# Optimization experiments

Measured on AMD Instinct MI355X. Metric: run time of the kernel, lower is better.

Reference implementation:

```python
import jax, jax.numpy as jnp
import numpy as np

H = 8
DH = 64
MAX_REL = 32
SCALE = DH ** -0.5


def setup_inputs() -> dict:
    key = jax.random.key(0)
    ks = jax.random.split(key, 10)
    B, T, D = 2, 2048, 512
    s = 1.0 / np.sqrt(D)
    return {
        "hidden_states": jax.random.normal(ks[0], (B, T, D), jnp.float32),
        "Wq": jax.random.normal(ks[1], (D, H * DH), jnp.float32) * s,
        "bq": jax.random.normal(ks[2], (H * DH,), jnp.float32) * 0.02,
        "Wk": jax.random.normal(ks[3], (D, H * DH), jnp.float32) * s,
        "bk": jax.random.normal(ks[4], (H * DH,), jnp.float32) * 0.02,
        "Wv": jax.random.normal(ks[5], (D, H * DH), jnp.float32) * s,
        "bv": jax.random.normal(ks[6], (H * DH,), jnp.float32) * 0.02,
        "Wo": jax.random.normal(ks[7], (H * DH, D), jnp.float32) * s,
        "bo": jax.random.normal(ks[8], (D,), jnp.float32) * 0.02,
        "rel_bias": jax.random.normal(ks[9], (H, 2 * MAX_REL + 1), jnp.float32) * 0.02,
    }


def _rel_pos_bias(rel_bias, Tq, Tk):
    # (H, Tq, Tk) additive bias from clamped relative distances
    rel = jnp.arange(Tq)[:, None] - jnp.arange(Tk)[None, :]
    idx = jnp.clip(rel, -MAX_REL, MAX_REL) + MAX_REL
    return rel_bias[:, idx]


def reference(hidden_states, Wq, bq, Wk, bk, Wv, bv, Wo, bo, rel_bias):
    B, T, D = hidden_states.shape
    # projections (enn.Linear == dense linear map in forward math)
    Q = (hidden_states @ Wq + bq).reshape(B, T, H, DH)
    K = (hidden_states @ Wk + bk).reshape(B, T, H, DH)
    V = (hidden_states @ Wv + bv).reshape(B, T, H, DH)
    attn = jnp.einsum("bthd,bkhd->bhtk", Q, K) * SCALE
    attn = attn + _rel_pos_bias(rel_bias, T, T)[None]
    attn = jax.nn.softmax(attn, axis=-1)
    out = jnp.einsum("bhtk,bkhd->bthd", attn, V).reshape(B, T, H * DH)
    return out @ Wo + bo
```

## Files before the change

kernel.cpp:

```cpp
#include <hip/hip_runtime.h>
#include <stdint.h>
#include <math.h>

#define H 8
#define DH 64
#define T 2048
#define D 512
#define B 2
#define BH 16
#define MAXREL 32
#define NREL (2*MAXREL+1)
#define C1 0.18033688f
#define NW (D*D)

typedef _Float16 half_t;
typedef half_t half8 __attribute__((ext_vector_type(8)));
typedef half_t half4 __attribute__((ext_vector_type(4)));
typedef float f32x4 __attribute__((ext_vector_type(4)));
typedef int int4v __attribute__((ext_vector_type(4)));

typedef __attribute__((address_space(3))) unsigned int lds_uint;
typedef const __attribute__((address_space(1))) unsigned int glb_uint;

__device__ __forceinline__ void gl_lds16(const void* g, void* l) {
    __builtin_amdgcn_global_load_lds((glb_uint*)g, (lds_uint*)l, 16, 0, 0);
}
__device__ __forceinline__ f32x4 zero4() { f32x4 z = {0.f,0.f,0.f,0.f}; return z; }
__device__ __forceinline__ int pkrtz(float a, float b) {
    return __builtin_bit_cast(int, __builtin_amdgcn_cvt_pkrtz(a, b));
}

__global__ __launch_bounds__(256) void prep(
    const float* __restrict__ X,
    const float* __restrict__ Wq, const float* __restrict__ Wk,
    const float* __restrict__ Wv, const float* __restrict__ Wo,
    half_t* __restrict__ Xh, half_t* __restrict__ Wts)
{
    __shared__ half_t Ld[64 * 72];
    const int bid = blockIdx.x;
    const int tid = threadIdx.x;
    if (bid < 1024) {
        const int i = (bid * 256 + tid) * 8;
        const float4 a = *(const float4*)(X + i);
        const float4 b = *(const float4*)(X + i + 4);
        half8 o;
        o[0]=(half_t)a.x; o[1]=(half_t)a.y; o[2]=(half_t)a.z; o[3]=(half_t)a.w;
        o[4]=(half_t)b.x; o[5]=(half_t)b.y; o[6]=(half_t)b.z; o[7]=(half_t)b.w;
        *(half8*)(Xh + i) = o;
    } else {
        const int id = bid - 1024;
        const int z = id >> 6;
        const int tile = id & 63;
        const float* __restrict__ W = (z==0)?Wq:(z==1)?Wk:(z==2)?Wv:Wo;
        half_t* __restrict__ out = Wts + (size_t)z * NW;
        const int k0 = (tile >> 3) * 64;
        const int n0 = (tile & 7) * 64;
        const int r = tid >> 2, c16 = (tid & 3) * 16;
        const float* src = W + (size_t)(k0 + r) * D + n0 + c16;
        #pragma unroll
        for (int j = 0; j < 16; ++j) Ld[r * 72 + c16 + j] = (half_t)src[j];
        __syncthreads();
        half_t tmp[16];
        #pragma unroll
        for (int j = 0; j < 16; ++j) tmp[j] = Ld[(c16 + j) * 72 + r];
        half8* dst = (half8*)(out + (size_t)(n0 + r) * D + k0 + c16);
        dst[0] = *(half8*)&tmp[0];
        dst[1] = *(half8*)&tmp[8];
    }
}

__global__ __launch_bounds__(256) void gemm_qkv(
    const half_t* __restrict__ Xh, const half_t* __restrict__ Wts,
    const float* __restrict__ bq, const float* __restrict__ bk,
    const float* __restrict__ bv,
    half_t* __restrict__ Qh, half_t* __restrict__ Kh, half_t* __restrict__ Vth)
{
    __shared__ half_t As[2][64 * 64];
    __shared__ half_t Bs[2][128 * 64];
    const int tid = threadIdx.x, w = tid >> 6, lane = tid & 63;
    const int l15 = lane & 15, quad = lane >> 4;
    const int m0 = blockIdx.x * 64, n0 = blockIdx.y * 128, z = blockIdx.z;
    const half_t* __restrict__ Wt = Wts + (size_t)z * NW;
    const float* __restrict__ bias = (z==0)?bq:(z==1)?bk:bv;

    auto stage = [&](int buf, int k0) {
        #pragma unroll
        for (int s = 0; s < 2; ++s) {
            const int cid = (w * 2 + s) * 64 + lane;
            const int r = cid >> 3, c = (cid & 7) ^ (r & 7);
            gl_lds16(Xh + (size_t)(m0 + r) * D + k0 + c * 8,
                     &As[buf][(w * 2 + s) * 512]);
        }
        #pragma unroll
        for (int s = 0; s < 4; ++s) {
            const int cid = (w * 4 + s) * 64 + lane;
            const int r = cid >> 3, c = (cid & 7) ^ (r & 7);
            gl_lds16(Wt + (size_t)(n0 + r) * D + k0 + c * 8,
                     &Bs[buf][(w * 4 + s) * 512]);
        }
    };

    f32x4 acc[4][2];
    #pragma unroll
    for (int ms = 0; ms < 4; ++ms) { acc[ms][0] = zero4(); acc[ms][1] = zero4(); }

    stage(0, 0);
    __syncthreads();
    for (int it = 0; it < 8; ++it) {
        const int cur = it & 1;
        if (it < 7) stage(cur ^ 1, (it + 1) * 64);
        const int swiz = l15 & 7;
        #pragma unroll
        for (int ks = 0; ks < 2; ++ks) {
            const int c = (ks * 4 + quad) ^ swiz;
            half8 bf[2];
            #pragma unroll
            for (int nt = 0; nt < 2; ++nt)
                bf[nt] = *(const half8*)&Bs[cur][(w * 32 + nt * 16 + l15) * 64 + c * 8];
            #pragma unroll
            for (int ms = 0; ms < 4; ++ms) {
                const half8 af = *(const half8*)&As[cur][(ms * 16 + l15) * 64 + c * 8];
                acc[ms][0] = __builtin_amdgcn_mfma_f32_16x16x32_f16(af, bf[0], acc[ms][0], 0, 0, 0);
                acc[ms][1] = __builtin_amdgcn_mfma_f32_16x16x32_f16(af, bf[1], acc[ms][1], 0, 0, 0);
            }
        }
        __syncthreads();
    }

    float bvv[2];
    #pragma unroll
    for (int nt = 0; nt < 2; ++nt) bvv[nt] = bias[n0 + w * 32 + nt * 16 + l15];

    if (z == 2) {
        #pragma unroll
        for (int ms = 0; ms < 4; ++ms) {
            const int mbase = m0 + ms * 16 + quad * 4;
            const int bb = mbase >> 11, t0 = mbase & 2047;
            #pragma unroll
            for (int nt = 0; nt < 2; ++nt) {
                const int n = n0 + w * 32 + nt * 16 + l15;
                const int hh = n >> 6, d = n & 63;
                half4 pk;
                #pragma unroll
                for (int r = 0; r < 4; ++r) pk[r] = (half_t)(acc[ms][nt][r] + bvv[nt]);
                *(half4*)(Vth + (((size_t)bb * H + hh) * DH + d) * T + t0) = pk;
            }
        }
    } else {
        half_t* __restrict__ dst = (z == 0) ? Qh : Kh;
        #pragma unroll
        for (int ms = 0; ms < 4; ++ms)
            #pragma unroll
            for (int nt = 0; nt < 2; ++nt)
                #pragma unroll
                for (int r = 0; r < 4; ++r) {
                    const int mrow = m0 + ms * 16 + quad * 4 + r;
                    const int n = n0 + w * 32 + nt * 16 + l15;
                    const int bb = mrow >> 11, t = mrow & 2047, hh = n >> 6, d = n & 63;
                    dst[(((size_t)bb * H + hh) * T + t) * DH + d] = (half_t)(acc[ms][nt][r] + bvv[nt]);
                }
    }
}

__global__ __launch_bounds__(256) void attn_fwd(
    const half_t* __restrict__ Qh, const half_t* __restrict__ Kh,
    const half_t* __restrict__ Vth, const float* __restrict__ relb,
    half_t* __restrict__ Onum, half_t* __restrict__ lsum)
{
    __shared__ half_t Kt[2][4096];
    __shared__ half_t Vt[2][4096];
    __shared__ float rb2[NREL];

    const int tid = threadIdx.x, w = tid >> 6, lane = tid & 63;
    const int l15 = lane & 15, quad = lane >> 4;
    const int q0 = blockIdx.x * 64;
    const int qw = q0 + w * 16;
    const int bh = blockIdx.y;
    const int split = blockIdx.z;
    const int kb0 = split * 1024;
    const int h = bh & 7;

    if (tid < NREL) rb2[tid] = relb[h * NREL + tid] * 1.44269504f;

    half8 qf[2];
    const half_t* Qbase = Qh + ((size_t)bh * T + qw) * DH;
    #pragma unroll
    for (int ks = 0; ks < 2; ++ks)
        qf[ks] = *(const half8*)(Qbase + l15 * DH + ks * 32 + quad * 8);

    f32x4 of[4];
    #pragma unroll
    for (int nt = 0; nt < 4; ++nt) of[nt] = zero4();
    float lp = 0.f;

    auto stage = [&](int buf, int kb) {
        #pragma unroll
        for (int s = 0; s < 2; ++s) {
            const int cid = (w * 2 + s) * 64 + lane;
            const int r = cid >> 3, cg = (cid & 7) ^ (r & 7);
            gl_lds16(Kh + ((size_t)bh * T + kb + r) * DH + cg * 8,
                     &Kt[buf][(w * 2 + s) * 512]);
            gl_lds16(Vth + ((size_t)bh * DH + r) * T + kb + cg * 8,
                     &Vt[buf][(w * 2 + s) * 512]);
        }
    };

    stage(0, kb0);
    __syncthreads();

    const int qg = qw + l15;
    const int swiz = l15 & 7;

    for (int it = 0; it < 16; ++it) {
        const int cur = it & 1;
        if (it + 1 < 16) stage(cur ^ 1, kb0 + (it + 1) * 64);
        const int kb = kb0 + it * 64;

        f32x4 st[4];
        #pragma unroll
        for (int nt = 0; nt < 4; ++nt) st[nt] = zero4();
        #pragma unroll
        for (int ks = 0; ks < 2; ++ks) {
            const int c = (ks * 4 + quad) ^ swiz;
            #pragma unroll
            for (int nt = 0; nt < 4; ++nt) {
                const half8 kf = *(const half8*)&Kt[cur][(nt * 16 + l15) * 64 + c * 8];
                st[nt] = __builtin_amdgcn_mfma_f32_16x16x32_f16(kf, qf[ks], st[nt], 0, 0, 0);
            }
        }

        int pd[4][2];
        const bool uni_hi = (qw - (kb + 63)) >= MAXREL;
        const bool uni_lo = ((qw + 15) - kb) <= -MAXREL;
        if (uni_hi || uni_lo) {
            const float bu = uni_hi ? rb2[NREL - 1] : rb2[0];
            #pragma unroll
            for (int nt = 0; nt < 4; ++nt) {
                float p[4];
                #pragma unroll
                for (int r = 0; r < 4; ++r) p[r] = exp2f(fmaf(st[nt][r], C1, bu));
                lp += (p[0] + p[1]) + (p[2] + p[3]);
                pd[nt][0] = pkrtz(p[0], p[1]);
                pd[nt][1] = pkrtz(p[2], p[3]);
            }
        } else {
            #pragma unroll
            for (int nt = 0; nt < 4; ++nt) {
                float p[4];
                #pragma unroll
                for (int r = 0; r < 4; ++r) {
                    const int key = kb + nt * 16 + quad * 4 + r;
                    int rel = qg - key;
                    rel = rel < -MAXREL ? -MAXREL : (rel > MAXREL ? MAXREL : rel);
                    p[r] = exp2f(fmaf(st[nt][r], C1, rb2[rel + MAXREL]));
                }
                lp += (p[0] + p[1]) + (p[2] + p[3]);
                pd[nt][0] = pkrtz(p[0], p[1]);
                pd[nt][1] = pkrtz(p[2], p[3]);
            }
        }

        #pragma unroll
        for (int ks = 0; ks < 2; ++ks) {
            int4v bd;
            #pragma unroll
            for (int d = 0; d < 4; ++d) {
                const int src = ((quad & 1) * 2 + (d >> 1)) * 16 + l15;
                const int va = __shfl(pd[2 * ks][d & 1], src);
                const int vb = __shfl(pd[2 * ks + 1][d & 1], src);
                bd[d] = (quad >> 1) ? vb : va;
            }
            const half8 pf = __builtin_bit_cast(half8, bd);
            const int c = (ks * 4 + quad) ^ swiz;
            #pragma unroll
            for (int nt = 0; nt < 4; ++nt) {
                const half8 vf = *(const half8*)&Vt[cur][(nt * 16 + l15) * 64 + c * 8];
                of[nt] = __builtin_amdgcn_mfma_f32_16x16x32_f16(vf, pf, of[nt], 0, 0, 0);
            }
        }
        __syncthreads();
    }

    const size_t qrow = (size_t)(split * BH + bh) * T + qw + l15;
    half_t* obase = Onum + qrow * DH;
    #pragma unroll
    for (int nt = 0; nt < 4; ++nt) {
        half4 pk;
        #pragma unroll
        for (int r = 0; r < 4; ++r) pk[r] = (half_t)(of[nt][r] * 0.015625f);
        *(half4*)(obase + nt * 16 + quad * 4) = pk;
    }
    lp += __shfl_xor(lp, 16);
    lp += __shfl_xor(lp, 32);
    if (quad == 0) lsum[qrow] = (half_t)(lp * 0.015625f);
}

__global__ __launch_bounds__(256) void combine(
    const half_t* __restrict__ Onum, const half_t* __restrict__ lsum,
    half_t* __restrict__ AOh)
{
    const int i = blockIdx.x * 256 + threadIdx.x;
    const int r = i >> 6;
    const int c = (i & 63) * 8;
    const int b = r >> 11, t = r & 2047, hh = c >> 6, d = c & 63;
    const int bh = b * H + hh;
    const size_t o0 = ((size_t)bh * T + t) * DH + d;
    const size_t o1 = ((size_t)(BH + bh) * T + t) * DH + d;
    const half8 x0 = *(const half8*)(Onum + o0);
    const half8 x1 = *(const half8*)(Onum + o1);
    const float l = (float)lsum[(size_t)bh * T + t] + (float)lsum[(size_t)(BH + bh) * T + t];
    const float inv = 1.0f / l;
    half8 o;
    #pragma unroll
    for (int j = 0; j < 8; ++j) o[j] = (half_t)(((float)x0[j] + (float)x1[j]) * inv);
    *(half8*)(AOh + (size_t)r * D + c) = o;
}

__global__ __launch_bounds__(256) void gemm_out(
    const half_t* __restrict__ AOh, const half_t* __restrict__ Wot,
    const float* __restrict__ bo, float* __restrict__ out)
{
    __shared__ half_t As[2][32 * 64];
    __shared__ half_t Bs[2][128 * 64];
    const int tid = threadIdx.x, w = tid >> 6, lane = tid & 63;
    const int l15 = lane & 15, quad = lane >> 4;
    const int m0 = blockIdx.x * 32, n0 = blockIdx.y * 128;

    auto stage = [&](int buf, int k0) {
        {
            const int cid = w * 64 + lane;
            const int r = cid >> 3, c = (cid & 7) ^ (r & 7);
            gl_lds16(AOh + (size_t)(m0 + r) * D + k0 + c * 8,
                     &As[buf][w * 512]);
        }
        #pragma unroll
        for (int s = 0; s < 4; ++s) {
            const int cid = (w * 4 + s) * 64 + lane;
            const int r = cid >> 3, c = (cid & 7) ^ (r & 7);
            gl_lds16(Wot + (size_t)(n0 + r) * D + k0 + c * 8,
                     &Bs[buf][(w * 4 + s) * 512]);
        }
    };

    f32x4 acc[2][2];
    #pragma unroll
    for (int ms = 0; ms < 2; ++ms) { acc[ms][0] = zero4(); acc[ms][1] = zero4(); }

    stage(0, 0);
    __syncthreads();
    for (int it = 0; it < 8; ++it) {
        const int cur = it & 1;
        if (it < 7) stage(cur ^ 1, (it + 1) * 64);
        const int swiz = l15 & 7;
        #pragma unroll
        for (int ks = 0; ks < 2; ++ks) {
            const int c = (ks * 4 + quad) ^ swiz;
            half8 bf[2];
            #pragma unroll
            for (int nt = 0; nt < 2; ++nt)
                bf[nt] = *(const half8*)&Bs[cur][(w * 32 + nt * 16 + l15) * 64 + c * 8];
            #pragma unroll
            for (int ms = 0; ms < 2; ++ms) {
                const half8 af = *(const half8*)&As[cur][(ms * 16 + l15) * 64 + c * 8];
                acc[ms][0] = __builtin_amdgcn_mfma_f32_16x16x32_f16(af, bf[0], acc[ms][0], 0, 0, 0);
                acc[ms][1] = __builtin_amdgcn_mfma_f32_16x16x32_f16(af, bf[1], acc[ms][1], 0, 0, 0);
            }
        }
        __syncthreads();
    }

    float bvv[2];
    #pragma unroll
    for (int nt = 0; nt < 2; ++nt) bvv[nt] = bo[n0 + w * 32 + nt * 16 + l15];
    #pragma unroll
    for (int ms = 0; ms < 2; ++ms)
        #pragma unroll
        for (int nt = 0; nt < 2; ++nt)
            #pragma unroll
            for (int r = 0; r < 4; ++r) {
                const int mrow = m0 + ms * 16 + quad * 4 + r;
                const int n = n0 + w * 32 + nt * 16 + l15;
                out[(size_t)mrow * D + n] = acc[ms][nt][r] + bvv[nt];
            }
}

extern "C" void kernel_launch(void* const* d_in, const int* in_sizes, int n_in,
                              void* d_out, int out_size, void* d_ws, size_t ws_size,
                              hipStream_t stream)
{
    const float* hs   = (const float*)d_in[0];
    const float* Wq   = (const float*)d_in[1];
    const float* bq   = (const float*)d_in[2];
    const float* Wk   = (const float*)d_in[3];
    const float* bk   = (const float*)d_in[4];
    const float* Wv   = (const float*)d_in[5];
    const float* bv   = (const float*)d_in[6];
    const float* Wo   = (const float*)d_in[7];
    const float* bo   = (const float*)d_in[8];
    const float* relb = (const float*)d_in[9];

    const size_t NX = (size_t)B * T * D;
    half_t* wsh = (half_t*)d_ws;
    half_t* Xh  = wsh;
    half_t* Wts = Xh + NX;
    half_t* Qh  = Wts + 4 * (size_t)NW;
    half_t* Kh  = Qh + NX;
    half_t* Vth = Kh + NX;
    half_t* On  = Vth + NX;
    half_t* Ls  = On + 2 * NX;
    half_t* AOh = Ls + 2 * BH * T;

    prep    <<<dim3(1280), 256, 0, stream>>>(hs, Wq, Wk, Wv, Wo, Xh, Wts);
    gemm_qkv<<<dim3(64, 4, 3), 256, 0, stream>>>(Xh, Wts, bq, bk, bv, Qh, Kh, Vth);
    attn_fwd<<<dim3(32, BH, 2), 256, 0, stream>>>(Qh, Kh, Vth, relb, On, Ls);
    combine <<<dim3(1024), 256, 0, stream>>>(On, Ls, AOh);
    gemm_out<<<dim3(128, 4), 256, 0, stream>>>(AOh, Wts + 3 * (size_t)NW, bo, (float*)d_out);
}
```

Before: 147.4 us.

## Process two query tiles per wave and split keys four ways in attention

Each wave now handles 32 query rows (two 16-row groups), so every K/V fragment read from LDS feeds two MFMAs. This cuts LDS traffic per unit of work. The key dimension is split four ways instead of two, which keeps the grid at the same 1024 blocks. Partial outputs go to two buffers, one of which reuses the output buffer, and the combine kernel reads the input-cast buffer as its destination. In exchange, register pressure rises under the new occupancy hint, and the combine step has more partials to read.

```diff
diff --git a/kernel.cpp b/kernel.cpp
--- a/kernel.cpp
+++ b/kernel.cpp
@@ -12,6 +12,8 @@
 #define NREL (2*MAXREL+1)
 #define C1 0.18033688f
 #define NW (D*D)
+#define NSPLIT 4
+#define NKIT (T/NSPLIT/64)
 
 typedef _Float16 half_t;
 typedef half_t half8 __attribute__((ext_vector_type(8)));
@@ -162,10 +164,11 @@
     }
 }
 
-__global__ __launch_bounds__(256) void attn_fwd(
+__global__ __launch_bounds__(256, 4) void attn_fwd(
     const half_t* __restrict__ Qh, const half_t* __restrict__ Kh,
     const half_t* __restrict__ Vth, const float* __restrict__ relb,
-    half_t* __restrict__ Onum, half_t* __restrict__ lsum)
+    half_t* __restrict__ On01, half_t* __restrict__ On23,
+    half_t* __restrict__ lsum)
 {
     __shared__ half_t Kt[2][4096];
     __shared__ half_t Vt[2][4096];
@@ -173,25 +176,28 @@
 
     const int tid = threadIdx.x, w = tid >> 6, lane = tid & 63;
     const int l15 = lane & 15, quad = lane >> 4;
-    const int q0 = blockIdx.x * 64;
-    const int qw = q0 + w * 16;
+    const int qw = blockIdx.x * 128 + w * 32;
     const int bh = blockIdx.y;
     const int split = blockIdx.z;
-    const int kb0 = split * 1024;
+    const int kb0 = split * (T / NSPLIT);
     const int h = bh & 7;
 
     if (tid < NREL) rb2[tid] = relb[h * NREL + tid] * 1.44269504f;
 
-    half8 qf[2];
+    half8 qf[2][2];
     const half_t* Qbase = Qh + ((size_t)bh * T + qw) * DH;
     #pragma unroll
-    for (int ks = 0; ks < 2; ++ks)
-        qf[ks] = *(const half8*)(Qbase + l15 * DH + ks * 32 + quad * 8);
-
-    f32x4 of[4];
-    #pragma unroll
-    for (int nt = 0; nt < 4; ++nt) of[nt] = zero4();
-    float lp = 0.f;
+    for (int g = 0; g < 2; ++g)
+        #pragma unroll
+        for (int ks = 0; ks < 2; ++ks)
+            qf[g][ks] = *(const half8*)(Qbase + (g * 16 + l15) * DH + ks * 32 + quad * 8);
+
+    f32x4 of[2][4];
+    #pragma unroll
+    for (int g = 0; g < 2; ++g)
+        #pragma unroll
+        for (int nt = 0; nt < 4; ++nt) of[g][nt] = zero4();
+    float lp[2] = {0.f, 0.f};
 
     auto stage = [&](int buf, int kb) {
         #pragma unroll
@@ -208,111 +214,137 @@
     stage(0, kb0);
     __syncthreads();
 
-    const int qg = qw + l15;
     const int swiz = l15 & 7;
 
-    for (int it = 0; it < 16; ++it) {
+    for (int it = 0; it < NKIT; ++it) {
         const int cur = it & 1;
-        if (it + 1 < 16) stage(cur ^ 1, kb0 + (it + 1) * 64);
+        if (it + 1 < NKIT) stage(cur ^ 1, kb0 + (it + 1) * 64);
         const int kb = kb0 + it * 64;
 
-        f32x4 st[4];
-        #pragma unroll
-        for (int nt = 0; nt < 4; ++nt) st[nt] = zero4();
+        f32x4 st[2][4];
+        #pragma unroll
+        for (int g = 0; g < 2; ++g)
+            #pragma unroll
+            for (int nt = 0; nt < 4; ++nt) st[g][nt] = zero4();
         #pragma unroll
         for (int ks = 0; ks < 2; ++ks) {
             const int c = (ks * 4 + quad) ^ swiz;
             #pragma unroll
             for (int nt = 0; nt < 4; ++nt) {
                 const half8 kf = *(const half8*)&Kt[cur][(nt * 16 + l15) * 64 + c * 8];
-                st[nt] = __builtin_amdgcn_mfma_f32_16x16x32_f16(kf, qf[ks], st[nt], 0, 0, 0);
-            }
-        }
-
-        int pd[4][2];
+                st[0][nt] = __builtin_amdgcn_mfma_f32_16x16x32_f16(kf, qf[0][ks], st[0][nt], 0, 0, 0);
+                st[1][nt] = __builtin_amdgcn_mfma_f32_16x16x32_f16(kf, qf[1][ks], st[1][nt], 0, 0, 0);
+            }
+        }
+
+        int pd[2][4][2];
         const bool uni_hi = (qw - (kb + 63)) >= MAXREL;
-        const bool uni_lo = ((qw + 15) - kb) <= -MAXREL;
+        const bool uni_lo = ((qw + 31) - kb) <= -MAXREL;
         if (uni_hi || uni_lo) {
             const float bu = uni_hi ? rb2[NREL - 1] : rb2[0];
             #pragma unroll
-            for (int nt = 0; nt < 4; ++nt) {
-                float p[4];
+            for (int g = 0; g < 2; ++g)
                 #pragma unroll
-                for (int r = 0; r < 4; ++r) p[r] = exp2f(fmaf(st[nt][r], C1, bu));
-                lp += (p[0] + p[1]) + (p[2] + p[3]);
-                pd[nt][0] = pkrtz(p[0], p[1]);
-                pd[nt][1] = pkrtz(p[2], p[3]);
-            }
+                for (int nt = 0; nt < 4; ++nt) {
+                    float p[4];
+                    #pragma unroll
+                    for (int r = 0; r < 4; ++r) p[r] = exp2f(fmaf(st[g][nt][r], C1, bu));
+                    lp[g] += (p[0] + p[1]) + (p[2] + p[3]);
+                    pd[g][nt][0] = pkrtz(p[0], p[1]);
+                    pd[g][nt][1] = pkrtz(p[2], p[3]);
+                }
         } else {
             #pragma unroll
-            for (int nt = 0; nt < 4; ++nt) {
-                float p[4];
+            for (int g = 0; g < 2; ++g) {
+                const int qg = qw + g * 16 + l15;
                 #pragma unroll
-                for (int r = 0; r < 4; ++r) {
-                    const int key = kb + nt * 16 + quad * 4 + r;
-                    int rel = qg - key;
-                    rel = rel < -MAXREL ? -MAXREL : (rel > MAXREL ? MAXREL : rel);
-                    p[r] = exp2f(fmaf(st[nt][r], C1, rb2[rel + MAXREL]));
+                for (int nt = 0; nt < 4; ++nt) {
+                    float p[4];
+                    #pragma unroll
+                    for (int r = 0; r < 4; ++r) {
+                        const int key = kb + nt * 16 + quad * 4 + r;
+                        int rel = qg - key;
+                        rel = rel < -MAXREL ? -MAXREL : (rel > MAXREL ? MAXREL : rel);
+                        p[r] = exp2f(fmaf(st[g][nt][r], C1, rb2[rel + MAXREL]));
+                    }
+                    lp[g] += (p[0] + p[1]) + (p[2] + p[3]);
+                    pd[g][nt][0] = pkrtz(p[0], p[1]);
+                    pd[g][nt][1] = pkrtz(p[2], p[3]);
                 }
-                lp += (p[0] + p[1]) + (p[2] + p[3]);
-                pd[nt][0] = pkrtz(p[0], p[1]);
-                pd[nt][1] = pkrtz(p[2], p[3]);
             }
         }
 
         #pragma unroll
         for (int ks = 0; ks < 2; ++ks) {
-            int4v bd;
-            #pragma unroll
-            for (int d = 0; d < 4; ++d) {
-                const int src = ((quad & 1) * 2 + (d >> 1)) * 16 + l15;
-                const int va = __shfl(pd[2 * ks][d & 1], src);
-                const int vb = __shfl(pd[2 * ks + 1][d & 1], src);
-                bd[d] = (quad >> 1) ? vb : va;
-            }
-            const half8 pf = __builtin_bit_cast(half8, bd);
+            half8 pf[2];
+            #pragma unroll
+            for (int g = 0; g < 2; ++g) {
+                int4v bd;
+                #pragma unroll
+                for (int d = 0; d < 4; ++d) {
+                    const int src = ((quad & 1) * 2 + (d >> 1)) * 16 + l15;
+                    const int va = __shfl(pd[g][2 * ks][d & 1], src);
+                    const int vb = __shfl(pd[g][2 * ks + 1][d & 1], src);
+                    bd[d] = (quad >> 1) ? vb : va;
+                }
+                pf[g] = __builtin_bit_cast(half8, bd);
+            }
             const int c = (ks * 4 + quad) ^ swiz;
             #pragma unroll
             for (int nt = 0; nt < 4; ++nt) {
                 const half8 vf = *(const half8*)&Vt[cur][(nt * 16 + l15) * 64 + c * 8];
-                of[nt] = __builtin_amdgcn_mfma_f32_16x16x32_f16(vf, pf, of[nt], 0, 0, 0);
+                of[0][nt] = __builtin_amdgcn_mfma_f32_16x16x32_f16(vf, pf[0], of[0][nt], 0, 0, 0);
+                of[1][nt] = __builtin_amdgcn_mfma_f32_16x16x32_f16(vf, pf[1], of[1][nt], 0, 0, 0);
             }
         }
         __syncthreads();
     }
 
-    const size_t qrow = (size_t)(split * BH + bh) * T + qw + l15;
-    half_t* obase = Onum + qrow * DH;
-    #pragma unroll
-    for (int nt = 0; nt < 4; ++nt) {
-        half4 pk;
-        #pragma unroll
-        for (int r = 0; r < 4; ++r) pk[r] = (half_t)(of[nt][r] * 0.015625f);
-        *(half4*)(obase + nt * 16 + quad * 4) = pk;
-    }
-    lp += __shfl_xor(lp, 16);
-    lp += __shfl_xor(lp, 32);
-    if (quad == 0) lsum[qrow] = (half_t)(lp * 0.015625f);
+    half_t* Obuf = (split < 2) ? On01 : On23;
+    const int sl = split & 1;
+    #pragma unroll
+    for (int g = 0; g < 2; ++g) {
+        const size_t qrow = ((size_t)(sl * BH + bh)) * T + qw + g * 16 + l15;
+        half_t* obase = Obuf + qrow * DH;
+        #pragma unroll
+        for (int nt = 0; nt < 4; ++nt) {
+            half4 pk;
+            #pragma unroll
+            for (int r = 0; r < 4; ++r) pk[r] = (half_t)(of[g][nt][r] * 0.015625f);
+            *(half4*)(obase + nt * 16 + quad * 4) = pk;
+        }
+        float v = lp[g];
+        v += __shfl_xor(v, 16);
+        v += __shfl_xor(v, 32);
+        if (quad == 0)
+            lsum[((size_t)(split * BH + bh)) * T + qw + g * 16 + l15] = (half_t)(v * 0.015625f);
+    }
 }
 
 __global__ __launch_bounds__(256) void combine(
-    const half_t* __restrict__ Onum, const half_t* __restrict__ lsum,
-    half_t* __restrict__ AOh)
+    const half_t* __restrict__ On01, const half_t* __restrict__ On23,
+    const half_t* __restrict__ lsum, half_t* __restrict__ AOh)
 {
     const int i = blockIdx.x * 256 + threadIdx.x;
     const int r = i >> 6;
     const int c = (i & 63) * 8;
     const int b = r >> 11, t = r & 2047, hh = c >> 6, d = c & 63;
     const int bh = b * H + hh;
-    const size_t o0 = ((size_t)bh * T + t) * DH + d;
-    const size_t o1 = ((size_t)(BH + bh) * T + t) * DH + d;
-    const half8 x0 = *(const half8*)(Onum + o0);
-    const half8 x1 = *(const half8*)(Onum + o1);
-    const float l = (float)lsum[(size_t)bh * T + t] + (float)lsum[(size_t)(BH + bh) * T + t];
+    float acc[8] = {};
+    float l = 0.f;
+    #pragma unroll
+    for (int s = 0; s < NSPLIT; ++s) {
+        const half_t* Obuf = (s < 2) ? On01 : On23;
+        const size_t off = ((size_t)((s & 1) * BH + bh) * T + t) * DH + d;
+        const half8 x = *(const half8*)(Obuf + off);
+        #pragma unroll
+        for (int j = 0; j < 8; ++j) acc[j] += (float)x[j];
+        l += (float)lsum[(size_t)(s * BH + bh) * T + t];
+    }
     const float inv = 1.0f / l;
     half8 o;
     #pragma unroll
-    for (int j = 0; j < 8; ++j) o[j] = (half_t)(((float)x0[j] + (float)x1[j]) * inv);
+    for (int j = 0; j < 8; ++j) o[j] = (half_t)(acc[j] * inv);
     *(half8*)(AOh + (size_t)r * D + c) = o;
 }
 
@@ -406,13 +438,14 @@
     half_t* Qh  = Wts + 4 * (size_t)NW;
     half_t* Kh  = Qh + NX;
     half_t* Vth = Kh + NX;
-    half_t* On  = Vth + NX;
-    half_t* Ls  = On + 2 * NX;
-    half_t* AOh = Ls + 2 * BH * T;
+    half_t* On23 = Vth + NX;
+    half_t* Ls  = On23 + 2 * NX;
+    half_t* On01 = (half_t*)d_out;
+    half_t* AOh = Xh;
 
     prep    <<<dim3(1280), 256, 0, stream>>>(hs, Wq, Wk, Wv, Wo, Xh, Wts);
     gemm_qkv<<<dim3(64, 4, 3), 256, 0, stream>>>(Xh, Wts, bq, bk, bv, Qh, Kh, Vth);
-    attn_fwd<<<dim3(32, BH, 2), 256, 0, stream>>>(Qh, Kh, Vth, relb, On, Ls);
-    combine <<<dim3(1024), 256, 0, stream>>>(On, Ls, AOh);
+    attn_fwd<<<dim3(16, BH, NSPLIT), 256, 0, stream>>>(Qh, Kh, Vth, relb, On01, On23, Ls);
+    combine <<<dim3(1024), 256, 0, stream>>>(On01, On23, Ls, AOh);
     gemm_out<<<dim3(128, 4), 256, 0, stream>>>(AOh, Wts + 3 * (size_t)NW, bo, (float*)d_out);
 }
```

Measured after the change: 153.5 us. +4.1%, slower.
